# Kernel tuning notes

Hardware: AMD Instinct MI355X
Metric: run time of the kernel (lower is better)

Reference implementation:

```python
import jax, jax.numpy as jnp
import numpy as np

K = 16  # neighbors, incl. self


def setup_inputs() -> dict:
    key = jax.random.key(0)
    ks = jax.random.split(key, 16)
    N, C = 8192, 256  # points, channels (inter_channels == in_channels == C)
    s = 0.05
    inp = {
        'coords': jax.random.uniform(ks[0], (N, 3), dtype=jnp.float32) * 100.0,
        'feats': jax.random.normal(ks[1], (N, C), dtype=jnp.float32),
        'theta_w': jax.random.normal(ks[2], (C, C), dtype=jnp.float32) * s,
        'theta_b': jax.random.normal(ks[3], (C,), dtype=jnp.float32) * s,
        'phi_w': jax.random.normal(ks[4], (C, C), dtype=jnp.float32) * s,
        'phi_b': jax.random.normal(ks[5], (C,), dtype=jnp.float32) * s,
        'g_w': jax.random.normal(ks[6], (C, C), dtype=jnp.float32) * s,
        'g_b': jax.random.normal(ks[7], (C,), dtype=jnp.float32) * s,
        'pe1_w1': jax.random.normal(ks[8], (3, C), dtype=jnp.float32) * s,
        'pe1_b1': jax.random.normal(ks[9], (C,), dtype=jnp.float32) * s,
        'pe1_w2': jax.random.normal(ks[10], (C, C), dtype=jnp.float32) * s,
        'pe1_b2': jax.random.normal(ks[11], (C,), dtype=jnp.float32) * s,
        'W_w': jax.random.normal(ks[12], (C, C), dtype=jnp.float32) * s,
        'W_b': jax.random.normal(ks[13], (C,), dtype=jnp.float32) * s,
    }
    return inp


def reference(coords, feats, theta_w, theta_b, phi_w, phi_b, g_w, g_b,
              pe1_w1, pe1_b1, pe1_w2, pe1_b2, W_w, W_b):
    C = feats.shape[-1]
    # KNN (squared dists, includes self as nearest) == pytorch3d knn_points
    sq = jnp.sum(coords * coords, axis=-1)  # [N]
    d2 = sq[:, None] + sq[None, :] - 2.0 * (coords @ coords.T)  # [N,N]
    _, idx = jax.lax.top_k(-d2, K)  # [N,K] sorted by ascending distance

    nn_coords = coords[idx]            # [N,K,3] knn gather
    nn_feats = feats[idx]              # [N,K,C]

    theta_f = feats @ theta_w + theta_b          # [N,C]
    phi_f = nn_feats @ phi_w + phi_b             # [N,K,C]

    delta_coords = nn_coords - coords[:, None, :]  # [N,K,3]
    # pe1 MLP; NOTE: original code uses pe1 for both pe1 and pe2 (shared)
    pe = jax.nn.relu(delta_coords @ pe1_w1 + pe1_b1) @ pe1_w2 + pe1_b2  # [N,K,C]

    delta_features = (pe * (theta_f[:, None, :] - phi_f) + pe) / jnp.sqrt(jnp.float32(C))
    sim = jax.nn.softmax(delta_features, axis=1)  # softmax over K neighbors

    g_feats = nn_feats @ g_w + g_b               # [N,K,C]
    y = jnp.sum(sim * g_feats, axis=1)           # [N,C]

    # W (1x1 Minkowski conv == per-point linear) + residual
    return y @ W_w + W_b + feats
```

## Files before the change

kernel.cpp:

```cpp
#include <hip/hip_runtime.h>

typedef __bf16 bf16_t;
typedef bf16_t bf16x8 __attribute__((ext_vector_type(8)));
typedef bf16_t bf16x4 __attribute__((ext_vector_type(4)));
typedef bf16_t bf16x2 __attribute__((ext_vector_type(2)));
typedef float f32x4 __attribute__((ext_vector_type(4)));
typedef unsigned long long u64;

#define N_PTS 8192
#define C_DIM 256
#define K_NN 16

#define GRID_G    16
#define GRID_NC   (GRID_G * GRID_G * GRID_G)
#define GRID_CELL 6.25f
#define GRID_INV  0.16f

#define CAST_NBLK 2048
#define PREPW_NBLK 320
__global__ __launch_bounds__(256) void prep_kernel(
    const float* __restrict__ feats, bf16_t* __restrict__ fb,
    const float* __restrict__ w0, const float* __restrict__ w1,
    const float* __restrict__ w2, const float* __restrict__ w3,
    const float* __restrict__ w4, bf16_t* __restrict__ wt_base,
    int* __restrict__ cellCount, int* __restrict__ gcount) {
    const int b = blockIdx.x;
    const int t = threadIdx.x;

    if (b < CAST_NBLK) {
        int i = (b * 256 + t) * 4;
        float4 v = *(const float4*)(feats + i);
        bf16x4 o;
        o[0] = (bf16_t)v.x; o[1] = (bf16_t)v.y; o[2] = (bf16_t)v.z; o[3] = (bf16_t)v.w;
        *(bf16x4*)(fb + i) = o;
    } else if (b < CAST_NBLK + PREPW_NBLK) {
        int pb = b - CAST_NBLK;
        int m = pb >> 6;
        int bx = pb & 63;
        const float* src = (m == 0) ? w0 : (m == 1) ? w1 : (m == 2) ? w2 : (m == 3) ? w3 : w4;
        bf16_t* dst = wt_base + m * (C_DIM * C_DIM);
#pragma unroll
        for (int i = 0; i < 4; ++i) {
            int o = bx * 1024 + i * 256 + t;
            int tkb = o >> 9;
            int rem = o & 511;
            int lm = rem >> 5;
            int r = rem & 31;
            int k = (tkb & 7) * 32 + r;
            int n = (tkb >> 3) * 16 + lm;
            dst[o] = (bf16_t)src[k * C_DIM + n];
        }
    } else {
        int zb = b - CAST_NBLK - PREPW_NBLK;
        cellCount[zb * 256 + t] = 0;
        if (zb == 0 && t == 0) *gcount = 0;
    }
}

__global__ __launch_bounds__(256) void grid_count_kernel(const float* __restrict__ coords,
                                                         int* __restrict__ cellCount,
                                                         int* __restrict__ cid) {
    int i = blockIdx.x * 256 + threadIdx.x;
    float x = coords[3 * i + 0], y = coords[3 * i + 1], z = coords[3 * i + 2];
    int cx = (int)(x * GRID_INV); if (cx > GRID_G - 1) cx = GRID_G - 1;
    int cy = (int)(y * GRID_INV); if (cy > GRID_G - 1) cy = GRID_G - 1;
    int cz = (int)(z * GRID_INV); if (cz > GRID_G - 1) cz = GRID_G - 1;
    int c = (cx * GRID_G + cy) * GRID_G + cz;
    cid[i] = c;
    atomicAdd(&cellCount[c], 1);
}

__global__ __launch_bounds__(256) void grid_scan_kernel(const int* __restrict__ cellCount,
                                                        int* __restrict__ cellStart,
                                                        int* __restrict__ cellPtr) {
    __shared__ int part[256];
    int t = threadIdx.x;
    int base = t * 16;
    int v[16];
    int sum = 0;
#pragma unroll
    for (int i = 0; i < 16; ++i) { v[i] = cellCount[base + i]; sum += v[i]; }
    part[t] = sum;
    __syncthreads();
    for (int off = 1; off < 256; off <<= 1) {
        int x = (t >= off) ? part[t - off] : 0;
        __syncthreads();
        part[t] += x;
        __syncthreads();
    }
    int acc = part[t] - sum;
#pragma unroll
    for (int i = 0; i < 16; ++i) {
        cellStart[base + i] = acc;
        cellPtr[base + i] = acc;
        acc += v[i];
    }
    if (t == 255) cellStart[GRID_NC] = acc;
}

__global__ __launch_bounds__(256) void grid_scatter_kernel(
    const float* __restrict__ coords, const int* __restrict__ cid, int* __restrict__ cellPtr,
    float* __restrict__ sx, float* __restrict__ sy, float* __restrict__ sz,
    float* __restrict__ ssq, int* __restrict__ sidx) {
    int i = blockIdx.x * 256 + threadIdx.x;
    int c = cid[i];
    int pos = atomicAdd(&cellPtr[c], 1);
    float x = coords[3 * i + 0], y = coords[3 * i + 1], z = coords[3 * i + 2];
    sx[pos] = x; sy[pos] = y; sz[pos] = z;
    ssq[pos] = __fadd_rn(__fadd_rn(__fmul_rn(x, x), __fmul_rn(y, y)), __fmul_rn(z, z));
    sidx[pos] = i;
}

__global__ __launch_bounds__(256) void knn_grid_kernel(
    const float* __restrict__ coords, const int* __restrict__ cellStart,
    const float* __restrict__ sx, const float* __restrict__ sy,
    const float* __restrict__ sz, const float* __restrict__ ssq,
    const int* __restrict__ sidx,
    int* __restrict__ idx_out, int* __restrict__ glist, int* __restrict__ gcount) {
    const int tid = threadIdx.x;
    const int wave = tid >> 6, lane = tid & 63;
    const int q = blockIdx.x * 4 + wave;

    __shared__ int segBase[4][25];
    __shared__ int segPref[4][26];
    __shared__ u64 cand[4][256];
    __shared__ int cnt[4];

    if (lane == 0) cnt[wave] = 0;

    const float qx = coords[3 * q + 0], qy = coords[3 * q + 1], qz = coords[3 * q + 2];
    const float sqi = __fadd_rn(__fadd_rn(__fmul_rn(qx, qx), __fmul_rn(qy, qy)),
                                __fmul_rn(qz, qz));

    int cx = (int)(qx * GRID_INV); if (cx > GRID_G - 1) cx = GRID_G - 1;
    int cy = (int)(qy * GRID_INV); if (cy > GRID_G - 1) cy = GRID_G - 1;
    int cz = (int)(qz * GRID_INV); if (cz > GRID_G - 1) cz = GRID_G - 1;
    int wx0 = cx - 2; if (wx0 < 0) wx0 = 0;
    int wx1 = cx + 2; if (wx1 > GRID_G - 1) wx1 = GRID_G - 1;
    int wy0 = cy - 2; if (wy0 < 0) wy0 = 0;
    int wy1 = cy + 2; if (wy1 > GRID_G - 1) wy1 = GRID_G - 1;
    int wz0 = cz - 2; if (wz0 < 0) wz0 = 0;
    int wz1 = cz + 2; if (wz1 > GRID_G - 1) wz1 = GRID_G - 1;

    const float INF = __int_as_float(0x7f800000);
    float rc = INF;
    if (wx0 > 0)          rc = fminf(rc, qx - (float)wx0 * GRID_CELL);
    if (wx1 < GRID_G - 1) rc = fminf(rc, (float)(wx1 + 1) * GRID_CELL - qx);
    if (wy0 > 0)          rc = fminf(rc, qy - (float)wy0 * GRID_CELL);
    if (wy1 < GRID_G - 1) rc = fminf(rc, (float)(wy1 + 1) * GRID_CELL - qy);
    if (wz0 > 0)          rc = fminf(rc, qz - (float)wz0 * GRID_CELL);
    if (wz1 < GRID_G - 1) rc = fminf(rc, (float)(wz1 + 1) * GRID_CELL - qz);
    float rc2 = rc * rc * 0.9999f;

    int nx = wx1 - wx0 + 1, nyc = wy1 - wy0 + 1;
    int ns = nx * nyc;
    if (lane < ns) {
        int scx = wx0 + lane / nyc;
        int scy = wy0 + lane % nyc;
        int b = (scx * GRID_G + scy) * GRID_G;
        int s0 = cellStart[b + wz0];
        int s1 = cellStart[b + wz1 + 1];
        segBase[wave][lane] = s0;
        segPref[wave][lane] = s1 - s0;
    }
    __syncthreads();
    if (lane == 0) {
        int acc = 0;
        for (int s = 0; s < ns; ++s) { int l = segPref[wave][s]; segPref[wave][s] = acc; acc += l; }
        segPref[wave][ns] = acc;
    }
    __syncthreads();

    const int M = segPref[wave][ns];
    bool flag = (M < K_NN);

    float lmin = INF;
    {
        int s = 0;
        for (int t = lane; t < M; t += 64) {
            while (t >= segPref[wave][s + 1]) ++s;
            int pos = segBase[wave][s] + (t - segPref[wave][s]);
            float x = sx[pos], y = sy[pos], z = sz[pos], sj = ssq[pos];
            float dot = __fmaf_rn(z, qz, __fmaf_rn(y, qy, __fmul_rn(x, qx)));
            float d2 = __fsub_rn(__fadd_rn(sqi, sj), __fmul_rn(2.0f, dot));
            lmin = fminf(lmin, d2);
        }
    }
    float g = fminf(lmin, __shfl_xor(lmin, 1));
    g = fminf(g, __shfl_xor(g, 2));
    float tau = fmaxf(g, __shfl_xor(g, 4));
    tau = fmaxf(tau, __shfl_xor(tau, 8));
    tau = fmaxf(tau, __shfl_xor(tau, 16));
    tau = fmaxf(tau, __shfl_xor(tau, 32));

    {
        int s = 0;
        for (int t = lane; t < M; t += 64) {
            while (t >= segPref[wave][s + 1]) ++s;
            int pos = segBase[wave][s] + (t - segPref[wave][s]);
            float x = sx[pos], y = sy[pos], z = sz[pos], sj = ssq[pos];
            float dot = __fmaf_rn(z, qz, __fmaf_rn(y, qy, __fmul_rn(x, qx)));
            float d2 = __fsub_rn(__fadd_rn(sqi, sj), __fmul_rn(2.0f, dot));
            if (d2 <= tau) {
                unsigned u = __float_as_uint(d2);
                u = (u & 0x80000000u) ? ~u : (u | 0x80000000u);
                int slot = atomicAdd(&cnt[wave], 1);
                if (slot < 256)
                    cand[wave][slot] = (((u64)u) << 32) | (unsigned)sidx[pos];
            }
        }
    }
    __syncthreads();

    int m = cnt[wave];
    if (m > 256) { flag = true; m = 256; }
    u64 k0 = ~0ull, k1 = ~0ull, k2 = ~0ull, k3 = ~0ull;
    if (lane < m) k0 = cand[wave][lane];
    if (lane + 64 < m) k1 = cand[wave][lane + 64];
    if (lane + 128 < m) k2 = cand[wave][lane + 128];
    if (lane + 192 < m) k3 = cand[wave][lane + 192];
    u64 lm2 = k0; int li = 0;
    if (k1 < lm2) { lm2 = k1; li = 1; }
    if (k2 < lm2) { lm2 = k2; li = 2; }
    if (k3 < lm2) { lm2 = k3; li = 3; }
    int keep = 0;
    u64 last = ~0ull;
#pragma unroll 1
    for (int r = 0; r < 16; ++r) {
        u64 w = lm2;
#pragma unroll
        for (int off = 1; off < 64; off <<= 1) {
            u64 o = __shfl_xor(w, off);
            w = (o < w) ? o : w;
        }
        if (lane == r) keep = (int)(unsigned)(w & 0xffffffffull);
        last = w;
        if (lm2 == w) {
            if (li == 0) k0 = ~0ull;
            else if (li == 1) k1 = ~0ull;
            else if (li == 2) k2 = ~0ull;
            else k3 = ~0ull;
            lm2 = k0; li = 0;
            if (k1 < lm2) { lm2 = k1; li = 1; }
            if (k2 < lm2) { lm2 = k2; li = 2; }
            if (k3 < lm2) { lm2 = k3; li = 3; }
        }
    }

    if (!flag) {
        unsigned ou = (unsigned)(last >> 32);
        unsigned db = (ou & 0x80000000u) ? (ou ^ 0x80000000u) : ~ou;
        float d16 = __uint_as_float(db);
        if (d16 >= rc2) flag = true;
    }
    if (flag && lane == 0) {
        int sl = atomicAdd(gcount, 1);
        glist[sl] = q;
    }
    if (lane < 16) idx_out[q * K_NN + lane] = keep;
}

__global__ __launch_bounds__(256) void knn_fallback_kernel(const float* __restrict__ coords,
                                                           const int* __restrict__ glist,
                                                           const int* __restrict__ gcount,
                                                           int* __restrict__ idx_out) {
    const int count = *gcount;
    const int n0 = blockIdx.x * 4;
    if (n0 >= count) return;

    const int tid = threadIdx.x;
    const int wave = tid >> 6, lane = tid & 63;
    __shared__ float red16[4][16];
    __shared__ u64 cand[4][256];
    __shared__ int cnt[4];
    __shared__ int qids[4];

    if (tid < 4) {
        cnt[tid] = 0;
        int slot = n0 + tid;
        qids[tid] = glist[slot < count ? slot : count - 1];
    }
    __syncthreads();

    float qx[4], qy[4], qz[4], sqi[4];
#pragma unroll
    for (int q = 0; q < 4; ++q) {
        int id = qids[q];
        qx[q] = coords[3 * id + 0];
        qy[q] = coords[3 * id + 1];
        qz[q] = coords[3 * id + 2];
        sqi[q] = __fadd_rn(__fadd_rn(__fmul_rn(qx[q], qx[q]), __fmul_rn(qy[q], qy[q])),
                           __fmul_rn(qz[q], qz[q]));
    }

    const float INF = __int_as_float(0x7f800000);
    const float* cp = coords + tid * 96;

    float lmin[4] = {INF, INF, INF, INF};
#pragma unroll
    for (int c = 0; c < 4; ++c) {
        float buf[24];
#pragma unroll
        for (int v = 0; v < 6; ++v)
            *(float4*)(buf + v * 4) = *(const float4*)(cp + c * 24 + v * 4);
#pragma unroll
        for (int p = 0; p < 8; ++p) {
            float x = buf[3 * p + 0], y = buf[3 * p + 1], z = buf[3 * p + 2];
            float sqj = __fadd_rn(__fadd_rn(__fmul_rn(x, x), __fmul_rn(y, y)),
                                  __fmul_rn(z, z));
#pragma unroll
            for (int q = 0; q < 4; ++q) {
                float dot = __fmaf_rn(z, qz[q], __fmaf_rn(y, qy[q], __fmul_rn(x, qx[q])));
                float d2 = __fsub_rn(__fadd_rn(sqi[q], sqj), __fmul_rn(2.0f, dot));
                lmin[q] = fminf(lmin[q], d2);
            }
        }
    }

#pragma unroll
    for (int q = 0; q < 4; ++q) {
        float g = lmin[q];
        g = fminf(g, __shfl_xor(g, 1));
        g = fminf(g, __shfl_xor(g, 2));
        g = fminf(g, __shfl_xor(g, 4));
        g = fminf(g, __shfl_xor(g, 8));
        if ((lane & 15) == 0) red16[q][wave * 4 + (lane >> 4)] = g;
    }
    __syncthreads();

    float tau[4];
#pragma unroll
    for (int q = 0; q < 4; ++q) {
        float t = red16[q][0];
#pragma unroll
        for (int i = 1; i < 16; ++i) t = fmaxf(t, red16[q][i]);
        tau[q] = t;
    }

#pragma unroll
    for (int c = 0; c < 4; ++c) {
        float buf[24];
#pragma unroll
        for (int v = 0; v < 6; ++v)
            *(float4*)(buf + v * 4) = *(const float4*)(cp + c * 24 + v * 4);
#pragma unroll
        for (int p = 0; p < 8; ++p) {
            float x = buf[3 * p + 0], y = buf[3 * p + 1], z = buf[3 * p + 2];
            float sqj = __fadd_rn(__fadd_rn(__fmul_rn(x, x), __fmul_rn(y, y)),
                                  __fmul_rn(z, z));
            int j = tid * 32 + c * 8 + p;
#pragma unroll
            for (int q = 0; q < 4; ++q) {
                float dot = __fmaf_rn(z, qz[q], __fmaf_rn(y, qy[q], __fmul_rn(x, qx[q])));
                float d2 = __fsub_rn(__fadd_rn(sqi[q], sqj), __fmul_rn(2.0f, dot));
                if (d2 <= tau[q]) {
                    unsigned u = __float_as_uint(d2);
                    u = (u & 0x80000000u) ? ~u : (u | 0x80000000u);
                    int slot = atomicAdd(&cnt[q], 1);
                    if (slot < 256)
                        cand[q][slot] = (((u64)u) << 32) | (unsigned)j;
                }
            }
        }
    }
    __syncthreads();

    int m = cnt[wave]; if (m > 256) m = 256;
    u64 k0 = ~0ull, k1 = ~0ull, k2 = ~0ull, k3 = ~0ull;
    if (lane < m) k0 = cand[wave][lane];
    if (lane + 64 < m) k1 = cand[wave][lane + 64];
    if (lane + 128 < m) k2 = cand[wave][lane + 128];
    if (lane + 192 < m) k3 = cand[wave][lane + 192];
    u64 lm2 = k0; int li = 0;
    if (k1 < lm2) { lm2 = k1; li = 1; }
    if (k2 < lm2) { lm2 = k2; li = 2; }
    if (k3 < lm2) { lm2 = k3; li = 3; }
    int keep = 0;
#pragma unroll 1
    for (int r = 0; r < 16; ++r) {
        u64 w = lm2;
#pragma unroll
        for (int off = 1; off < 64; off <<= 1) {
            u64 o = __shfl_xor(w, off);
            w = (o < w) ? o : w;
        }
        if (lane == r) keep = (int)(unsigned)(w & 0xffffffffull);
        if (lm2 == w) {
            if (li == 0) k0 = ~0ull;
            else if (li == 1) k1 = ~0ull;
            else if (li == 2) k2 = ~0ull;
            else k3 = ~0ull;
            lm2 = k0; li = 0;
            if (k1 < lm2) { lm2 = k1; li = 1; }
            if (k2 < lm2) { lm2 = k2; li = 2; }
            if (k3 < lm2) { lm2 = k3; li = 3; }
        }
    }
    if (lane < 16) idx_out[qids[wave] * K_NN + lane] = keep;
}

__global__ __launch_bounds__(256, 2) void proj_kernel(
    const bf16_t* __restrict__ fb, const bf16_t* __restrict__ wt_base,
    const float* __restrict__ tb, const float* __restrict__ pb, const float* __restrict__ gb,
    float* __restrict__ T, bf16_t* __restrict__ PG) {
    const int sel = blockIdx.y;
    const bf16_t* Wt = wt_base + sel * (C_DIM * C_DIM);
    const float* bias = (sel == 0) ? tb : (sel == 1) ? pb : gb;
    const int wave = threadIdx.x >> 6, lane = threadIdx.x & 63;
    const int q = lane >> 4, lm = lane & 15;
    const int m0 = blockIdx.x * 64;

    bf16x8 bfr[4][8];
#pragma unroll
    for (int ti = 0; ti < 4; ++ti)
#pragma unroll
        for (int kb = 0; kb < 8; ++kb)
            bfr[ti][kb] = *(const bf16x8*)(Wt + (((wave * 4 + ti) * 8 + kb) << 9) + lm * 32 + q * 8);

    float bv[4];
#pragma unroll
    for (int ti = 0; ti < 4; ++ti) bv[ti] = bias[(wave * 4 + ti) * 16 + lm];

#pragma unroll
    for (int p = 0; p < 4; ++p) {
        const bf16_t* arow = fb + (m0 + p * 16 + lm) * C_DIM + q * 8;
        bf16x8 a[8];
#pragma unroll
        for (int kb = 0; kb < 8; ++kb) a[kb] = *(const bf16x8*)(arow + kb * 32);
        f32x4 acc[4];
#pragma unroll
        for (int ti = 0; ti < 4; ++ti) acc[ti] = (f32x4){0.f, 0.f, 0.f, 0.f};
#pragma unroll
        for (int ti = 0; ti < 4; ++ti)
#pragma unroll
            for (int kb = 0; kb < 8; ++kb)
                acc[ti] = __builtin_amdgcn_mfma_f32_16x16x32_bf16(a[kb], bfr[ti][kb], acc[ti], 0, 0, 0);

#pragma unroll
        for (int ti = 0; ti < 4; ++ti) {
            int c = (wave * 4 + ti) * 16 + lm;
#pragma unroll
            for (int r = 0; r < 4; ++r) {
                float v = acc[ti][r] + bv[ti];
                int off = (m0 + p * 16 + q * 4 + r) * C_DIM + c;
                if (sel == 0) T[off] = v;
                else if (sel == 1) PG[2 * off] = (bf16_t)v;
                else PG[2 * off + 1] = (bf16_t)v;
            }
        }
    }
}

#define HPAD 264
#define P_BLK 8
#define HROWS (P_BLK * 16)
__global__ __launch_bounds__(256, 2) void pe2_fused_kernel(
    const float* __restrict__ coords, const int* __restrict__ idx,
    const float* __restrict__ T, const bf16_t* __restrict__ PG,
    const float* __restrict__ w1, const float* __restrict__ b1, const float* __restrict__ b2,
    const bf16_t* __restrict__ Wt2, const bf16_t* __restrict__ Wt3,
    const float* __restrict__ Wb, const float* __restrict__ feats,
    float* __restrict__ out) {
    __shared__ __align__(16) bf16_t h_lds[HROWS * HPAD];
    __shared__ __align__(16) bf16_t yl[16][HPAD];
    __shared__ float dxyz[HROWS][3];
    __shared__ int idxl[HROWS];
    const int tid = threadIdx.x;
    const int p0 = blockIdx.x * P_BLK;
    const int wave = tid >> 6, lane = tid & 63;
    const int q = lane >> 4, lm = lane & 15;

    bf16x8 bfr[4][8];
#pragma unroll
    for (int ti = 0; ti < 4; ++ti)
#pragma unroll
        for (int kb = 0; kb < 8; ++kb)
            bfr[ti][kb] = *(const bf16x8*)(Wt2 + (((wave * 4 + ti) * 8 + kb) << 9) + lm * 32 + q * 8);
    float b2c[4];
#pragma unroll
    for (int ti = 0; ti < 4; ++ti) b2c[ti] = b2[(wave * 4 + ti) * 16 + lm];

    {
        bf16x8 z8 = (bf16x8){(bf16_t)0.f, (bf16_t)0.f, (bf16_t)0.f, (bf16_t)0.f,
                             (bf16_t)0.f, (bf16_t)0.f, (bf16_t)0.f, (bf16_t)0.f};
        *(bf16x8*)(&yl[8 + (tid >> 5)][(tid & 31) * 8]) = z8;
    }

    if (tid < HROWS) {
        int n = p0 + (tid >> 4);
        int j = idx[n * K_NN + (tid & 15)];
        idxl[tid] = j;
        dxyz[tid][0] = coords[3 * j + 0] - coords[3 * n + 0];
        dxyz[tid][1] = coords[3 * j + 1] - coords[3 * n + 1];
        dxyz[tid][2] = coords[3 * j + 2] - coords[3 * n + 2];
    }
    __syncthreads();

    {
        int c = tid;
        float wx = w1[c], wy = w1[C_DIM + c], wz = w1[2 * C_DIM + c], bb = b1[c];
#pragma unroll 4
        for (int r = 0; r < HROWS; ++r) {
            float pre = dxyz[r][0] * wx + dxyz[r][1] * wy + dxyz[r][2] * wz + bb;
            h_lds[r * HPAD + c] = (bf16_t)fmaxf(pre, 0.0f);
        }
    }
    __syncthreads();

#pragma unroll 1
    for (int lp = 0; lp < P_BLK; ++lp) {
        const int n = p0 + lp;

        int jr[4];
#pragma unroll
        for (int r = 0; r < 4; ++r) jr[r] = idxl[lp * 16 + q * 4 + r];
        bf16x2 pg[4][4];
        float Tn[4];
#pragma unroll
        for (int ti = 0; ti < 4; ++ti) {
            int c = (wave * 4 + ti) * 16 + lm;
            Tn[ti] = T[n * C_DIM + c];
#pragma unroll
            for (int r = 0; r < 4; ++r)
                pg[ti][r] = *(const bf16x2*)(PG + 2 * (jr[r] * C_DIM + c));
        }

        const bf16_t* hrow = h_lds + (lp * 16 + lm) * HPAD + q * 8;
        bf16x8 a[8];
#pragma unroll
        for (int kb = 0; kb < 8; ++kb) a[kb] = *(const bf16x8*)(hrow + kb * 32);
        f32x4 acc[4];
#pragma unroll
        for (int ti = 0; ti < 4; ++ti) acc[ti] = (f32x4){0.f, 0.f, 0.f, 0.f};
#pragma unroll
        for (int ti = 0; ti < 4; ++ti)
#pragma unroll
            for (int kb = 0; kb < 8; ++kb)
                acc[ti] = __builtin_amdgcn_mfma_f32_16x16x32_bf16(a[kb], bfr[ti][kb], acc[ti], 0, 0, 0);

#pragma unroll
        for (int ti = 0; ti < 4; ++ti) {
            int c = (wave * 4 + ti) * 16 + lm;
            float df[4];
#pragma unroll
            for (int r = 0; r < 4; ++r) {
                float pe = acc[ti][r] + b2c[ti];
                df[r] = (pe * (Tn[ti] - (float)pg[ti][r][0]) + pe) * 0.0625f;
            }
            float mx = fmaxf(fmaxf(df[0], df[1]), fmaxf(df[2], df[3]));
            mx = fmaxf(mx, __shfl_xor(mx, 16));
            mx = fmaxf(mx, __shfl_xor(mx, 32));
            float e[4], s = 0.f;
#pragma unroll
            for (int r = 0; r < 4; ++r) { e[r] = __expf(df[r] - mx); s += e[r]; }
            s += __shfl_xor(s, 16);
            s += __shfl_xor(s, 32);
            float inv = 1.0f / s;
            float y = 0.f;
#pragma unroll
            for (int r = 0; r < 4; ++r) y += e[r] * inv * (float)pg[ti][r][1];
            y += __shfl_xor(y, 16);
            y += __shfl_xor(y, 32);
            if (q == 0) yl[lp][c] = (bf16_t)y;
        }
    }
    __syncthreads();

#pragma unroll
    for (int ti = 0; ti < 4; ++ti)
#pragma unroll
        for (int kb = 0; kb < 8; ++kb)
            bfr[ti][kb] = *(const bf16x8*)(Wt3 + (((wave * 4 + ti) * 8 + kb) << 9) + lm * 32 + q * 8);
    float bw[4];
#pragma unroll
    for (int ti = 0; ti < 4; ++ti) bw[ti] = Wb[(wave * 4 + ti) * 16 + lm];

    bf16x8 a2[8];
#pragma unroll
    for (int kb = 0; kb < 8; ++kb) a2[kb] = *(const bf16x8*)(&yl[lm][kb * 32 + q * 8]);
    f32x4 acc2[4];
#pragma unroll
    for (int ti = 0; ti < 4; ++ti) acc2[ti] = (f32x4){0.f, 0.f, 0.f, 0.f};
#pragma unroll
    for (int ti = 0; ti < 4; ++ti)
#pragma unroll
        for (int kb = 0; kb < 8; ++kb)
            acc2[ti] = __builtin_amdgcn_mfma_f32_16x16x32_bf16(a2[kb], bfr[ti][kb], acc2[ti], 0, 0, 0);

#pragma unroll
    for (int ti = 0; ti < 4; ++ti) {
        int c = (wave * 4 + ti) * 16 + lm;
#pragma unroll
        for (int r = 0; r < 4; ++r) {
            int row = q * 4 + r;
            if (row < P_BLK) {
                int off = (p0 + row) * C_DIM + c;
                out[off] = acc2[ti][r] + bw[ti] + feats[off];
            }
        }
    }
}

extern "C" void kernel_launch(void* const* d_in, const int* in_sizes, int n_in,
                              void* d_out, int out_size, void* d_ws, size_t ws_size,
                              hipStream_t stream) {
    const float* coords = (const float*)d_in[0];
    const float* feats  = (const float*)d_in[1];
    const float* theta_w = (const float*)d_in[2];
    const float* theta_b = (const float*)d_in[3];
    const float* phi_w   = (const float*)d_in[4];
    const float* phi_b   = (const float*)d_in[5];
    const float* g_w     = (const float*)d_in[6];
    const float* g_b     = (const float*)d_in[7];
    const float* pe1_w1  = (const float*)d_in[8];
    const float* pe1_b1  = (const float*)d_in[9];
    const float* pe1_w2  = (const float*)d_in[10];
    const float* pe1_b2  = (const float*)d_in[11];
    const float* W_w     = (const float*)d_in[12];
    const float* W_b     = (const float*)d_in[13];
    float* out = (float*)d_out;

    char* w = (char*)d_ws;
    size_t off = 0;
    int* idx = (int*)(w + off);        off += (size_t)N_PTS * K_NN * 4;
    bf16_t* fb = (bf16_t*)(w + off);   off += (size_t)N_PTS * C_DIM * 2;
    bf16_t* wt = (bf16_t*)(w + off);   off += (size_t)5 * C_DIM * C_DIM * 2;
    float* T = (float*)(w + off);      off += (size_t)N_PTS * C_DIM * 4;
    bf16_t* PG = (bf16_t*)(w + off);   off += (size_t)N_PTS * C_DIM * 4;
    int* cid       = (int*)(w + off);  off += (size_t)N_PTS * 4;
    int* cellCount = (int*)(w + off);  off += (size_t)GRID_NC * 4;
    int* cellStart = (int*)(w + off);  off += (size_t)(GRID_NC + 1) * 4;
    int* cellPtr   = (int*)(w + off);  off += (size_t)GRID_NC * 4;
    float* sxp = (float*)(w + off);    off += (size_t)N_PTS * 4;
    float* syp = (float*)(w + off);    off += (size_t)N_PTS * 4;
    float* szp = (float*)(w + off);    off += (size_t)N_PTS * 4;
    float* ssqp = (float*)(w + off);   off += (size_t)N_PTS * 4;
    int* sidxp = (int*)(w + off);      off += (size_t)N_PTS * 4;
    int* glist = (int*)(w + off);      off += (size_t)N_PTS * 4;
    int* gcount = (int*)(w + off);     off += 256;
    (void)ws_size; (void)in_sizes; (void)n_in; (void)out_size;

    prep_kernel<<<CAST_NBLK + PREPW_NBLK + 16, 256, 0, stream>>>(
        feats, fb, theta_w, phi_w, g_w, pe1_w2, W_w, wt, cellCount, gcount);

    grid_count_kernel<<<N_PTS / 256, 256, 0, stream>>>(coords, cellCount, cid);
    grid_scan_kernel<<<1, 256, 0, stream>>>(cellCount, cellStart, cellPtr);
    grid_scatter_kernel<<<N_PTS / 256, 256, 0, stream>>>(coords, cid, cellPtr,
                                                         sxp, syp, szp, ssqp, sidxp);
    knn_grid_kernel<<<N_PTS / 4, 256, 0, stream>>>(coords, cellStart, sxp, syp, szp,
                                                   ssqp, sidxp, idx, glist, gcount);
    knn_fallback_kernel<<<N_PTS / 4, 256, 0, stream>>>(coords, glist, gcount, idx);

    proj_kernel<<<dim3(N_PTS / 64, 3), 256, 0, stream>>>(fb, wt, theta_b, phi_b, g_b, T, PG);
    pe2_fused_kernel<<<N_PTS / P_BLK, 256, 0, stream>>>(coords, idx, T, PG,
                                                        pe1_w1, pe1_b1, pe1_b2,
                                                        wt + 3 * C_DIM * C_DIM,
                                                        wt + 4 * C_DIM * C_DIM,
                                                        W_b, feats, out);
}
```

Baseline: 214.8 us.

## Split pe2 kernel by output-channel halves, double-buffer hidden, separate final GEMM

The fused pe2 kernel is split across two channel halves (grid y), so each wave holds half the pe1_w2 fragments and the launch bound rises to three blocks per CU. The hidden-layer LDS buffer shrinks to a two-slot ring computed one point ahead, replacing the full 128-row staging buffer. The W projection and residual move to a separate final_kernel that reads y from a new bf16 workspace buffer with 64-row tiles. The aim is higher occupancy and less LDS and register use, at the cost of recomputing the hidden layer in both halves, an extra global round trip for y, an extra launch, and a barrier per point.

```diff
diff --git a/kernel.cpp b/kernel.cpp
--- a/kernel.cpp
+++ b/kernel.cpp
@@ -454,37 +454,29 @@
 #define HPAD 264
 #define P_BLK 8
 #define HROWS (P_BLK * 16)
-__global__ __launch_bounds__(256, 2) void pe2_fused_kernel(
+__global__ __launch_bounds__(256, 3) void pe2_fused_kernel(
     const float* __restrict__ coords, const int* __restrict__ idx,
     const float* __restrict__ T, const bf16_t* __restrict__ PG,
     const float* __restrict__ w1, const float* __restrict__ b1, const float* __restrict__ b2,
-    const bf16_t* __restrict__ Wt2, const bf16_t* __restrict__ Wt3,
-    const float* __restrict__ Wb, const float* __restrict__ feats,
-    float* __restrict__ out) {
-    __shared__ __align__(16) bf16_t h_lds[HROWS * HPAD];
-    __shared__ __align__(16) bf16_t yl[16][HPAD];
+    const bf16_t* __restrict__ Wt2, bf16_t* __restrict__ yb) {
+    __shared__ __align__(16) bf16_t hbuf[2][16 * HPAD];
     __shared__ float dxyz[HROWS][3];
     __shared__ int idxl[HROWS];
     const int tid = threadIdx.x;
     const int p0 = blockIdx.x * P_BLK;
+    const int half = blockIdx.y;
     const int wave = tid >> 6, lane = tid & 63;
     const int q = lane >> 4, lm = lane & 15;
 
-    bf16x8 bfr[4][8];
-#pragma unroll
-    for (int ti = 0; ti < 4; ++ti)
+    bf16x8 bfr[2][8];
+#pragma unroll
+    for (int ti = 0; ti < 2; ++ti)
 #pragma unroll
         for (int kb = 0; kb < 8; ++kb)
-            bfr[ti][kb] = *(const bf16x8*)(Wt2 + (((wave * 4 + ti) * 8 + kb) << 9) + lm * 32 + q * 8);
-    float b2c[4];
-#pragma unroll
-    for (int ti = 0; ti < 4; ++ti) b2c[ti] = b2[(wave * 4 + ti) * 16 + lm];
-
-    {
-        bf16x8 z8 = (bf16x8){(bf16_t)0.f, (bf16_t)0.f, (bf16_t)0.f, (bf16_t)0.f,
-                             (bf16_t)0.f, (bf16_t)0.f, (bf16_t)0.f, (bf16_t)0.f};
-        *(bf16x8*)(&yl[8 + (tid >> 5)][(tid & 31) * 8]) = z8;
-    }
+            bfr[ti][kb] = *(const bf16x8*)(Wt2 + ((((half * 8 + wave * 2 + ti) * 8 + kb)) << 9) + lm * 32 + q * 8);
+    float b2c[2];
+#pragma unroll
+    for (int ti = 0; ti < 2; ++ti) b2c[ti] = b2[(half * 8 + wave * 2 + ti) * 16 + lm];
 
     if (tid < HROWS) {
         int n = p0 + (tid >> 4);
@@ -496,13 +488,13 @@
     }
     __syncthreads();
 
+    const float wx = w1[tid], wy = w1[C_DIM + tid], wz = w1[2 * C_DIM + tid], bb = b1[tid];
+
     {
-        int c = tid;
-        float wx = w1[c], wy = w1[C_DIM + c], wz = w1[2 * C_DIM + c], bb = b1[c];
-#pragma unroll 4
-        for (int r = 0; r < HROWS; ++r) {
+#pragma unroll
+        for (int r = 0; r < 16; ++r) {
             float pre = dxyz[r][0] * wx + dxyz[r][1] * wy + dxyz[r][2] * wz + bb;
-            h_lds[r * HPAD + c] = (bf16_t)fmaxf(pre, 0.0f);
+            hbuf[0][r * HPAD + tid] = (bf16_t)fmaxf(pre, 0.0f);
         }
     }
     __syncthreads();
@@ -510,37 +502,45 @@
 #pragma unroll 1
     for (int lp = 0; lp < P_BLK; ++lp) {
         const int n = p0 + lp;
+        const int cur = lp & 1;
 
         int jr[4];
 #pragma unroll
         for (int r = 0; r < 4; ++r) jr[r] = idxl[lp * 16 + q * 4 + r];
-        bf16x2 pg[4][4];
-        float Tn[4];
-#pragma unroll
-        for (int ti = 0; ti < 4; ++ti) {
-            int c = (wave * 4 + ti) * 16 + lm;
+        bf16x2 pg[2][4];
+        float Tn[2];
+#pragma unroll
+        for (int ti = 0; ti < 2; ++ti) {
+            int c = (half * 8 + wave * 2 + ti) * 16 + lm;
             Tn[ti] = T[n * C_DIM + c];
 #pragma unroll
             for (int r = 0; r < 4; ++r)
                 pg[ti][r] = *(const bf16x2*)(PG + 2 * (jr[r] * C_DIM + c));
         }
 
-        const bf16_t* hrow = h_lds + (lp * 16 + lm) * HPAD + q * 8;
-        bf16x8 a[8];
-#pragma unroll
-        for (int kb = 0; kb < 8; ++kb) a[kb] = *(const bf16x8*)(hrow + kb * 32);
-        f32x4 acc[4];
-#pragma unroll
-        for (int ti = 0; ti < 4; ++ti) acc[ti] = (f32x4){0.f, 0.f, 0.f, 0.f};
-#pragma unroll
-        for (int ti = 0; ti < 4; ++ti)
-#pragma unroll
-            for (int kb = 0; kb < 8; ++kb)
-                acc[ti] = __builtin_amdgcn_mfma_f32_16x16x32_bf16(a[kb], bfr[ti][kb], acc[ti], 0, 0, 0);
-
-#pragma unroll
-        for (int ti = 0; ti < 4; ++ti) {
-            int c = (wave * 4 + ti) * 16 + lm;
+        if (lp + 1 < P_BLK) {
+            int rb = (lp + 1) * 16;
+#pragma unroll
+            for (int r = 0; r < 16; ++r) {
+                float pre = dxyz[rb + r][0] * wx + dxyz[rb + r][1] * wy + dxyz[rb + r][2] * wz + bb;
+                hbuf[cur ^ 1][r * HPAD + tid] = (bf16_t)fmaxf(pre, 0.0f);
+            }
+        }
+
+        const bf16_t* hrow = &hbuf[cur][lm * HPAD + q * 8];
+        f32x4 acc[2];
+        acc[0] = (f32x4){0.f, 0.f, 0.f, 0.f};
+        acc[1] = (f32x4){0.f, 0.f, 0.f, 0.f};
+#pragma unroll
+        for (int kb = 0; kb < 8; ++kb) {
+            bf16x8 a = *(const bf16x8*)(hrow + kb * 32);
+            acc[0] = __builtin_amdgcn_mfma_f32_16x16x32_bf16(a, bfr[0][kb], acc[0], 0, 0, 0);
+            acc[1] = __builtin_amdgcn_mfma_f32_16x16x32_bf16(a, bfr[1][kb], acc[1], 0, 0, 0);
+        }
+
+#pragma unroll
+        for (int ti = 0; ti < 2; ++ti) {
+            int c = (half * 8 + wave * 2 + ti) * 16 + lm;
             float df[4];
 #pragma unroll
             for (int r = 0; r < 4; ++r) {
@@ -561,41 +561,52 @@
             for (int r = 0; r < 4; ++r) y += e[r] * inv * (float)pg[ti][r][1];
             y += __shfl_xor(y, 16);
             y += __shfl_xor(y, 32);
-            if (q == 0) yl[lp][c] = (bf16_t)y;
-        }
-    }
-    __syncthreads();
-
+            if (q == 0) yb[n * C_DIM + c] = (bf16_t)y;
+        }
+        __syncthreads();
+    }
+}
+
+__global__ __launch_bounds__(256, 2) void final_kernel(
+    const bf16_t* __restrict__ yb, const bf16_t* __restrict__ Wt,
+    const float* __restrict__ Wb, const float* __restrict__ feats,
+    float* __restrict__ out) {
+    const int wave = threadIdx.x >> 6, lane = threadIdx.x & 63;
+    const int q = lane >> 4, lm = lane & 15;
+    const int m0 = blockIdx.x * 64;
+
+    bf16x8 bfr[4][8];
 #pragma unroll
     for (int ti = 0; ti < 4; ++ti)
 #pragma unroll
         for (int kb = 0; kb < 8; ++kb)
-            bfr[ti][kb] = *(const bf16x8*)(Wt3 + (((wave * 4 + ti) * 8 + kb) << 9) + lm * 32 + q * 8);
-    float bw[4];
-#pragma unroll
-    for (int ti = 0; ti < 4; ++ti) bw[ti] = Wb[(wave * 4 + ti) * 16 + lm];
-
-    bf16x8 a2[8];
-#pragma unroll
-    for (int kb = 0; kb < 8; ++kb) a2[kb] = *(const bf16x8*)(&yl[lm][kb * 32 + q * 8]);
-    f32x4 acc2[4];
-#pragma unroll
-    for (int ti = 0; ti < 4; ++ti) acc2[ti] = (f32x4){0.f, 0.f, 0.f, 0.f};
-#pragma unroll
-    for (int ti = 0; ti < 4; ++ti)
-#pragma unroll
-        for (int kb = 0; kb < 8; ++kb)
-            acc2[ti] = __builtin_amdgcn_mfma_f32_16x16x32_bf16(a2[kb], bfr[ti][kb], acc2[ti], 0, 0, 0);
-
-#pragma unroll
-    for (int ti = 0; ti < 4; ++ti) {
-        int c = (wave * 4 + ti) * 16 + lm;
-#pragma unroll
-        for (int r = 0; r < 4; ++r) {
-            int row = q * 4 + r;
-            if (row < P_BLK) {
-                int off = (p0 + row) * C_DIM + c;
-                out[off] = acc2[ti][r] + bw[ti] + feats[off];
+            bfr[ti][kb] = *(const bf16x8*)(Wt + (((wave * 4 + ti) * 8 + kb) << 9) + lm * 32 + q * 8);
+    float bv[4];
+#pragma unroll
+    for (int ti = 0; ti < 4; ++ti) bv[ti] = Wb[(wave * 4 + ti) * 16 + lm];
+
+#pragma unroll
+    for (int p = 0; p < 4; ++p) {
+        const bf16_t* arow = yb + (m0 + p * 16 + lm) * C_DIM + q * 8;
+        bf16x8 a[8];
+#pragma unroll
+        for (int kb = 0; kb < 8; ++kb) a[kb] = *(const bf16x8*)(arow + kb * 32);
+        f32x4 acc[4];
+#pragma unroll
+        for (int ti = 0; ti < 4; ++ti) acc[ti] = (f32x4){0.f, 0.f, 0.f, 0.f};
+#pragma unroll
+        for (int ti = 0; ti < 4; ++ti)
+#pragma unroll
+            for (int kb = 0; kb < 8; ++kb)
+                acc[ti] = __builtin_amdgcn_mfma_f32_16x16x32_bf16(a[kb], bfr[ti][kb], acc[ti], 0, 0, 0);
+
+#pragma unroll
+        for (int ti = 0; ti < 4; ++ti) {
+            int c = (wave * 4 + ti) * 16 + lm;
+#pragma unroll
+            for (int r = 0; r < 4; ++r) {
+                int off = (m0 + p * 16 + q * 4 + r) * C_DIM + c;
+                out[off] = acc[ti][r] + bv[ti] + feats[off];
             }
         }
     }
@@ -627,6 +638,7 @@
     bf16_t* wt = (bf16_t*)(w + off);   off += (size_t)5 * C_DIM * C_DIM * 2;
     float* T = (float*)(w + off);      off += (size_t)N_PTS * C_DIM * 4;
     bf16_t* PG = (bf16_t*)(w + off);   off += (size_t)N_PTS * C_DIM * 4;
+    bf16_t* yb = (bf16_t*)(w + off);   off += (size_t)N_PTS * C_DIM * 2;
     int* cid       = (int*)(w + off);  off += (size_t)N_PTS * 4;
     int* cellCount = (int*)(w + off);  off += (size_t)GRID_NC * 4;
     int* cellStart = (int*)(w + off);  off += (size_t)(GRID_NC + 1) * 4;
@@ -652,9 +664,8 @@
     knn_fallback_kernel<<<N_PTS / 4, 256, 0, stream>>>(coords, glist, gcount, idx);
 
     proj_kernel<<<dim3(N_PTS / 64, 3), 256, 0, stream>>>(fb, wt, theta_b, phi_b, g_b, T, PG);
-    pe2_fused_kernel<<<N_PTS / P_BLK, 256, 0, stream>>>(coords, idx, T, PG,
-                                                        pe1_w1, pe1_b1, pe1_b2,
-                                                        wt + 3 * C_DIM * C_DIM,
-                                                        wt + 4 * C_DIM * C_DIM,
-                                                        W_b, feats, out);
-}
+    pe2_fused_kernel<<<dim3(N_PTS / P_BLK, 2), 256, 0, stream>>>(coords, idx, T, PG,
+                                                                 pe1_w1, pe1_b1, pe1_b2,
+                                                                 wt + 3 * C_DIM * C_DIM, yb);
+    final_kernel<<<N_PTS / 64, 256, 0, stream>>>(yb, wt + 4 * C_DIM * C_DIM, W_b, feats, out);
+}
```

Measured after the change: 209.7 us. 1.02x faster.
